# Kernel optimization log

Hardware: AMD Instinct MI355X
Metric: run time of the kernel (lower is better)

Reference implementation:

```python
import jax, jax.numpy as jnp
import numpy as np

TAG_SIZE = 50
START = TAG_SIZE - 2  # index of '<START>'
STOP = TAG_SIZE - 1   # index of '<STOP>'
B, S = 64, 512


def setup_inputs() -> dict:
    key = jax.random.key(0)
    k1, k2, k3 = jax.random.split(key, 3)
    feats = jax.random.normal(k1, (B, S, TAG_SIZE), dtype=jnp.float32)
    mask = jnp.ones((B, S), dtype=jnp.int32)
    tags = jax.random.randint(k2, (B, S), 0, START)  # valid tags exclude START/STOP
    transitions = jax.random.normal(k3, (TAG_SIZE, TAG_SIZE), dtype=jnp.float32)
    return {"feats": feats, "mask": mask, "tags": tags, "transitions": transitions}


def reference(feats, mask, tags, transitions):
    """CRF neg_log_likelihood_loss = forward_score (log partition, summed) - gold_score.
    feats: (B,S,T) emissions; mask: (B,S) {0,1}; tags: (B,S) gold tags;
    transitions[i,j] = score of transitioning from tag i to tag j.
    """
    b, s, t = feats.shape
    maskf = mask.astype(feats.dtype)

    # ---- forward algorithm (log partition) via scan over time ----
    feats_t = jnp.swapaxes(feats, 0, 1)            # (S,B,T)
    mask_t = jnp.swapaxes(mask, 0, 1).astype(bool)  # (S,B)
    # t=0: partition[b,j] = feats[b,0,j] + transitions[START, j]
    partition0 = feats_t[0] + transitions[START][None, :]  # (B,T)

    def step(partition, xs):
        f_t, m_t = xs  # (B,T), (B,)
        # cur_values[b,i,j] = partition[b,i] + transitions[i,j] + feats[b,t,j]
        cur_values = partition[:, :, None] + transitions[None, :, :] + f_t[:, None, :]
        cur = jax.nn.logsumexp(cur_values, axis=1)  # (B,T) logsumexp over prev tag
        new_partition = jnp.where(m_t[:, None], cur, partition)
        return new_partition, None

    partition, _ = jax.lax.scan(step, partition0, (feats_t[1:], mask_t[1:]))
    terminal = jax.nn.logsumexp(partition[:, :, None] + transitions[None, :, :], axis=1)  # (B,T)
    forward_score = terminal[:, STOP].sum()

    # ---- gold score ----
    # prev tag at step 0 is START, otherwise tags[:, t-1]
    prev = jnp.concatenate([jnp.full((b, 1), START, dtype=tags.dtype), tags[:, :-1]], axis=1)
    emit = jnp.take_along_axis(feats, tags[..., None], axis=2)[..., 0]  # (B,S)
    trans = transitions[prev, tags]                                      # (B,S)
    tg_energy = ((emit + trans) * maskf).sum()
    lengths = mask.astype(jnp.int32).sum(axis=1)                         # (B,)
    end_ids = jnp.take_along_axis(tags, (lengths - 1)[:, None].astype(tags.dtype), axis=1)[:, 0]
    end_energy = transitions[end_ids, STOP].sum()
    gold_score = tg_energy + end_energy

    return forward_score - gold_score
```

## Files before the change

### kernel.cpp

```cpp
#include <hip/hip_runtime.h>
#include <hip/hip_bf16.h>

#define T 50
#define NB 64
#define NS 512
#define START_TAG 48
#define STOP_TAG 49

typedef _Float16 f16_t;
typedef _Float16 f16x2 __attribute__((ext_vector_type(2)));
typedef _Float16 f16x4 __attribute__((ext_vector_type(4)));
typedef float    f32x4 __attribute__((ext_vector_type(4)));

static constexpr float LOG2E = 1.4426950408889634f;
static constexpr float LN2F  = 0.6931471805599453f;
static constexpr float S_E   = 6.0f;
#define NEG_BIG (-1.0e38f)

__device__ __forceinline__ float fexp2(float x) { return __builtin_amdgcn_exp2f(x); }
__device__ __forceinline__ float flog2(float x) { return __builtin_amdgcn_logf(x); }
__device__ __forceinline__ f16x2 bcast_h2(f16x2 v, int src) {
    unsigned u = __builtin_amdgcn_readlane(__builtin_bit_cast(unsigned, v), src);
    return __builtin_bit_cast(f16x2, u);
}
__device__ __forceinline__ f16x2 pack_h2(float a, float b) {
    return __builtin_bit_cast(f16x2, __builtin_amdgcn_cvt_pkrtz(a, b));
}

__device__ __forceinline__ float wave_fmax_dpp(float x) {
#define DPP_STEP(ctrl)                                                        \
    do {                                                                      \
        int _s = __builtin_bit_cast(int, x);                                  \
        int _p = __builtin_amdgcn_update_dpp(_s, _s, (ctrl), 0xf, 0xf, false);\
        x = fmaxf(x, __builtin_bit_cast(float, _p));                          \
    } while (0)
    DPP_STEP(0x111);
    DPP_STEP(0x112);
    DPP_STEP(0x114);
    DPP_STEP(0x118);
    DPP_STEP(0x142);
    DPP_STEP(0x143);
#undef DPP_STEP
    return __builtin_bit_cast(float,
        __builtin_amdgcn_readlane(__builtin_bit_cast(int, x), 63));
}

template<int NCHT, int CHLT>
__global__ __launch_bounds__(256, 6)
void crf_chunk(const float* __restrict__ feats, const int* __restrict__ mask,
               const float* __restrict__ trans, f16_t* __restrict__ wsCt,
               float* __restrict__ wsD, float* __restrict__ out, int out_size) {
    const int c    = blockIdx.x;
    const int b    = blockIdx.y;
    const int tid  = threadIdx.x;
    const int w    = tid >> 6;
    const int lane = tid & 63;
    const int l15  = lane & 15;
    const int q    = lane >> 4;

    __shared__ float sF[CHLT][64];
    __shared__ f16_t Ml[64 * 72];

    const int t0  = c * CHLT + 1;
    const int nst = (NS - t0 < CHLT) ? (NS - t0) : CHLT;

    f16x4 Afrag[4][4];
    #pragma unroll
    for (int mb = 0; mb < 4; mb++)
        #pragma unroll
        for (int kb = 0; kb < 4; kb++) {
            f16x4 v;
            #pragma unroll
            for (int j = 0; j < 4; j++) {
                const int kk = 16 * kb + 4 * q + j;
                const int mm = 16 * mb + l15;
                float x = 0.f;
                if (kk < T && mm < T) x = fexp2(fmaf(trans[kk * T + mm], LOG2E, -S_E));
                v[j] = (f16_t)x;
            }
            Afrag[mb][kb] = v;
        }

    for (int r = w; r < CHLT; r += 4) {
        int tl = t0 + r; tl = tl < NS ? tl : NS - 1;
        float fv = (lane < T && r < nst) ? feats[((size_t)b * NS + tl) * T + lane] : 0.f;
        sF[r][lane] = (lane < T && r < nst) ? fexp2(fv * LOG2E) : 0.f;
    }

    unsigned long long bm;
    {
        int tl = t0 + lane; tl = tl < NS ? tl : NS - 1;
        int mv = (lane < nst) ? mask[b * NS + tl] : 0;
        bm = __ballot(mv != 0);
    }
    __syncthreads();

    f16x4 Bt[4];
    #pragma unroll
    for (int rb = 0; rb < 4; rb++) {
        f16x4 v;
        #pragma unroll
        for (int j = 0; j < 4; j++)
            v[j] = (f16_t)((rb == w && 4 * q + j == l15) ? 1.f : 0.f);
        Bt[rb] = v;
    }

    float D  = 0.f;
    float m1 = 1.f, m2 = 1.f;

    for (int s = 0; s < nst; s++) {
        if ((bm >> s) & 1ull) {
            int ebits = (int)((__float_as_uint(m2) >> 23) & 255) - 127;
            ebits = ebits > 14 ? 14 : (ebits < -14 ? -14 : ebits);
            const float descale = __uint_as_float((unsigned)(127 - ebits) << 23);
            D += (float)ebits + S_E;

            const f32x4 zz = {0.f, 0.f, 0.f, 0.f};
            f32x4 acc[4];
            #pragma unroll
            for (int mb = 0; mb < 4; mb++)
                acc[mb] = __builtin_amdgcn_mfma_f32_16x16x16f16(Afrag[mb][0], Bt[0], zz, 0, 0, 0);
            #pragma unroll
            for (int kb = 1; kb < 4; kb++)
                #pragma unroll
                for (int mb = 0; mb < 4; mb++)
                    acc[mb] = __builtin_amdgcn_mfma_f32_16x16x16f16(Afrag[mb][kb], Bt[kb], acc[mb], 0, 0, 0);

            f16x2 wmax2 = {(f16_t)0.f, (f16_t)0.f};
            #pragma unroll
            for (int mb = 0; mb < 4; mb++) {
                f32x4 cs = *(const f32x4*)&sF[s][16 * mb + 4 * q];
                float v0 = acc[mb][0] * (cs[0] * descale);
                float v1 = acc[mb][1] * (cs[1] * descale);
                float v2 = acc[mb][2] * (cs[2] * descale);
                float v3 = acc[mb][3] * (cs[3] * descale);
                f16x4 hv;
                hv[0] = (f16_t)v0; hv[1] = (f16_t)v1;
                hv[2] = (f16_t)v2; hv[3] = (f16_t)v3;
                Bt[mb] = hv;
                f16x2 lo = __builtin_shufflevector(hv, hv, 0, 1);
                f16x2 hi = __builtin_shufflevector(hv, hv, 2, 3);
                wmax2 = __builtin_elementwise_max(wmax2,
                          __builtin_elementwise_max(lo, hi));
            }
            float wm = fmaxf((float)wmax2[0], (float)wmax2[1]);

            m2 = m1;
            m1 = wave_fmax_dpp(wm);
        }
    }

    {
        const int P2 = 72;
        #pragma unroll
        for (int rb = 0; rb < 4; rb++) {
            f16x4 v = Bt[rb];
            #pragma unroll
            for (int r = 0; r < 4; r++)
                Ml[(16 * rb + 4 * q + r) * P2 + 16 * w + l15] = v[r];
        }
        __syncthreads();
        const int row = tid >> 2;
        const int seg = tid & 3;
        const f16_t* src = &Ml[row * P2 + seg * 16];
        f16_t* dst = wsCt + ((size_t)(b * NCHT + c)) * 4096 + row * 64 + seg * 16;
        ((int4*)dst)[0] = *(const int4*)&src[0];
        ((int4*)dst)[1] = *(const int4*)&src[8];
    }
    if (lane == 0) wsD[(b * NCHT + c) * 4 + w] = D;

    if (c == 0 && b == 0 && tid < out_size) out[tid] = 0.f;
}

template<int NCHT>
__global__ __launch_bounds__(128, 1)
void crf_combine(const float* __restrict__ feats, const int* __restrict__ mask,
                 const int* __restrict__ tags, const float* __restrict__ trans,
                 const f16_t* __restrict__ wsCt, const float* __restrict__ wsD,
                 float* __restrict__ out) {
    const int b    = blockIdx.x;
    const int tid  = threadIdx.x;
    const int wv   = tid >> 6;
    const int lane = tid & 63;

    __shared__ float sGold;
    float fwd = 0.f;

    if (wv == 1) {
        float gsum = 0.f;
        int   lcnt = 0;
        for (int s = lane; s < NS; s += 64) {
            int   m  = mask[b * NS + s];
            int   tg = tags[b * NS + s];
            int   pv = (s == 0) ? START_TAG : tags[b * NS + s - 1];
            float e  = feats[((size_t)b * NS + s) * T + tg];
            float tr = trans[pv * T + tg];
            if (m) { gsum += e + tr; lcnt += 1; }
        }
        #pragma unroll
        for (int off = 32; off > 0; off >>= 1) {
            gsum += __shfl_down(gsum, off, 64);
            lcnt += __shfl_down(lcnt, off, 64);
        }
        if (lane == 0) sGold = gsum + trans[tags[b * NS + lcnt - 1] * T + STOP_TAG];
    } else {
        float part = (lane < T)
            ? (feats[(size_t)b * NS * T + lane] + trans[START_TAG * T + lane]) * LOG2E
            : NEG_BIG;

        float Dq[NCHT];
        #pragma unroll
        for (int cc = 0; cc < NCHT; cc++)
            Dq[cc] = wsD[(b * NCHT + cc) * 4 + (lane >> 4)];

        int bufA[32], bufB[32];
        {
            const f16_t* src = wsCt + (size_t)b * NCHT * 4096 + lane * 64;
            #pragma unroll
            for (int kk = 0; kk < 8; kk++)
                *(int4*)&bufA[4 * kk] = ((const int4*)src)[kk];
        }

        auto cbody = [&](int (&cur)[32], int (&nxt)[32], int cc) {
            if (cc + 1 < NCHT) {
                const f16_t* src = wsCt + (size_t)(b * NCHT + cc + 1) * 4096 + lane * 64;
                #pragma unroll
                for (int kk = 0; kk < 8; kk++)
                    *(int4*)&nxt[4 * kk] = ((const int4*)src)[kk];
            }

            float tmp = part + Dq[cc];
            float sft = wave_fmax_dpp(tmp);
            float ex  = fexp2(tmp - sft);
            float exo = __shfl_xor(ex, 1, 64);
            f16x2 pk  = pack_h2(ex, exo);

            float a0 = 0.f, a1 = 0.f, a2 = 0.f, a3 = 0.f;
            #pragma unroll
            for (int k = 0; k < 25; k += 4) {
                a0 = __builtin_amdgcn_fdot2(bcast_h2(pk, 2 * k), __builtin_bit_cast(f16x2, cur[k]), a0, false);
                if (k + 1 < 25) a1 = __builtin_amdgcn_fdot2(bcast_h2(pk, 2 * (k + 1)), __builtin_bit_cast(f16x2, cur[k + 1]), a1, false);
                if (k + 2 < 25) a2 = __builtin_amdgcn_fdot2(bcast_h2(pk, 2 * (k + 2)), __builtin_bit_cast(f16x2, cur[k + 2]), a2, false);
                if (k + 3 < 25) a3 = __builtin_amdgcn_fdot2(bcast_h2(pk, 2 * (k + 3)), __builtin_bit_cast(f16x2, cur[k + 3]), a3, false);
            }
            part = sft + flog2((a0 + a1) + (a2 + a3));
        };

        #pragma unroll
        for (int pp = 0; pp < NCHT / 2; pp++) {
            cbody(bufA, bufB, 2 * pp);
            cbody(bufB, bufA, 2 * pp + 1);
        }

        float v = (lane < T) ? part + trans[lane * T + STOP_TAG] * LOG2E : NEG_BIG;
        float mx = wave_fmax_dpp(v);
        float ee = (lane < T) ? fexp2(v - mx) : 0.f;
        #pragma unroll
        for (int off = 32; off > 0; off >>= 1) ee += __shfl_xor(ee, off, 64);
        fwd = (mx + flog2(ee)) * LN2F;
    }

    __syncthreads();
    if (tid == 0) atomicAdd(out, fwd - sGold);
}

extern "C" void kernel_launch(void* const* d_in, const int* in_sizes, int n_in,
                              void* d_out, int out_size, void* d_ws, size_t ws_size,
                              hipStream_t stream) {
    const float* feats = (const float*)d_in[0];
    const int*   mask  = (const int*)d_in[1];
    const int*   tags  = (const int*)d_in[2];
    const float* trans = (const float*)d_in[3];
    float* out = (float*)d_out;


    const size_t matBytes16 = (size_t)NB * 16 * 4096 * sizeof(f16_t);
    const size_t need16     = matBytes16 + (size_t)NB * 16 * 4 * sizeof(float);

    if (ws_size >= need16) {
        f16_t* wsCt = (f16_t*)d_ws;
        float* wsD  = (float*)((char*)d_ws + matBytes16);
        crf_chunk<16, 32><<<dim3(16, NB), 256, 0, stream>>>(feats, mask, trans, wsCt, wsD, out, out_size);
        crf_combine<16><<<NB, 128, 0, stream>>>(feats, mask, tags, trans, wsCt, wsD, out);
    } else {
        const size_t matBytes8 = (size_t)NB * 8 * 4096 * sizeof(f16_t);
        f16_t* wsCt = (f16_t*)d_ws;
        float* wsD  = (float*)((char*)d_ws + matBytes8);
        crf_chunk<8, 64><<<dim3(8, NB), 256, 0, stream>>>(feats, mask, trans, wsCt, wsD, out, out_size);
        crf_combine<8><<<NB, 128, 0, stream>>>(feats, mask, tags, trans, wsCt, wsD, out);
    }
}
```

Before: 106.5 us.

## Move transition MFMA fragments to LDS and triple-buffer chunk combine loads

The 16 register-resident A fragments of exp(transitions) move into a shared-memory buffer, and each step now reloads them as packed 8-wide LDS reads. This frees VGPRs so launch bounds can rise from 6 to 8 waves per SIMD. The shared buffer is reused for the final transpose, which needs an extra barrier. The chunk-combine phase switches from double to triple buffering of workspace loads to hide more global latency. The cost is eight LDS reads on the serial per-step MFMA chain, which adds latency to every timestep.

Measured after the change: 106.6 us. No clear change (+0.0%).

```diff
diff --git a/kernel.cpp b/kernel.cpp
--- a/kernel.cpp
+++ b/kernel.cpp
@@ -10,6 +10,7 @@
 typedef _Float16 f16_t;
 typedef _Float16 f16x2 __attribute__((ext_vector_type(2)));
 typedef _Float16 f16x4 __attribute__((ext_vector_type(4)));
+typedef _Float16 f16x8 __attribute__((ext_vector_type(8)));
 typedef float    f32x4 __attribute__((ext_vector_type(4)));
 
 static constexpr float LOG2E = 1.4426950408889634f;
@@ -46,7 +47,7 @@
 }
 
 template<int NCHT, int CHLT>
-__global__ __launch_bounds__(256, 6)
+__global__ __launch_bounds__(256, 8)
 void crf_chunk(const float* __restrict__ feats, const int* __restrict__ mask,
                const float* __restrict__ trans, f16_t* __restrict__ wsCt,
                float* __restrict__ wsD, float* __restrict__ out, int out_size) {
@@ -58,28 +59,36 @@
     const int l15  = lane & 15;
     const int q    = lane >> 4;
 
-    __shared__ float sF[CHLT][64];
-    __shared__ f16_t Ml[64 * 72];
+    constexpr int EF_BYTES = 4 * 2 * 64 * 16;
+    constexpr int SF_BYTES = CHLT * 64 * 4;
+    constexpr int ML_BYTES = 64 * 72 * 2;
+    constexpr int SM_BYTES = (EF_BYTES + SF_BYTES) > ML_BYTES
+                           ? (EF_BYTES + SF_BYTES) : ML_BYTES;
+    __shared__ unsigned char smem[SM_BYTES];
+    f16_t* Ef = (f16_t*)smem;
+    float (*sF)[64] = (float (*)[64])(smem + EF_BYTES);
 
     const int t0  = c * CHLT + 1;
     const int nst = (NS - t0 < CHLT) ? (NS - t0) : CHLT;
 
-    f16x4 Afrag[4][4];
-    #pragma unroll
-    for (int mb = 0; mb < 4; mb++)
-        #pragma unroll
-        for (int kb = 0; kb < 4; kb++) {
-            f16x4 v;
+    for (int sidx = tid; sidx < 512; sidx += 256) {
+        const int kb  = sidx >> 7;
+        const int mbp = (sidx >> 6) & 1;
+        const int ln  = sidx & 63;
+        const int qq  = ln >> 4;
+        const int ll  = ln & 15;
+        f16_t* slot = Ef + sidx * 8;
+        #pragma unroll
+        for (int e = 0; e < 2; e++)
             #pragma unroll
             for (int j = 0; j < 4; j++) {
-                const int kk = 16 * kb + 4 * q + j;
-                const int mm = 16 * mb + l15;
+                const int kk = 16 * kb + 4 * qq + j;
+                const int mm = 16 * (2 * mbp + e) + ll;
                 float x = 0.f;
                 if (kk < T && mm < T) x = fexp2(fmaf(trans[kk * T + mm], LOG2E, -S_E));
-                v[j] = (f16_t)x;
-            }
-            Afrag[mb][kb] = v;
-        }
+                slot[e * 4 + j] = (f16_t)x;
+            }
+    }
 
     for (int r = w; r < CHLT; r += 4) {
         int tl = t0 + r; tl = tl < NS ? tl : NS - 1;
@@ -107,6 +116,7 @@
 
     float D  = 0.f;
     float m1 = 1.f, m2 = 1.f;
+    const f16x8* EfL = (const f16x8*)Ef;
 
     for (int s = 0; s < nst; s++) {
         if ((bm >> s) & 1ull) {
@@ -117,14 +127,23 @@
 
             const f32x4 zz = {0.f, 0.f, 0.f, 0.f};
             f32x4 acc[4];
-            #pragma unroll
-            for (int mb = 0; mb < 4; mb++)
-                acc[mb] = __builtin_amdgcn_mfma_f32_16x16x16f16(Afrag[mb][0], Bt[0], zz, 0, 0, 0);
-            #pragma unroll
-            for (int kb = 1; kb < 4; kb++)
-                #pragma unroll
-                for (int mb = 0; mb < 4; mb++)
-                    acc[mb] = __builtin_amdgcn_mfma_f32_16x16x16f16(Afrag[mb][kb], Bt[kb], acc[mb], 0, 0, 0);
+            {
+                f16x8 p0 = EfL[0 * 64 + lane];
+                f16x8 p1 = EfL[1 * 64 + lane];
+                acc[0] = __builtin_amdgcn_mfma_f32_16x16x16f16(__builtin_shufflevector(p0, p0, 0,1,2,3), Bt[0], zz, 0, 0, 0);
+                acc[1] = __builtin_amdgcn_mfma_f32_16x16x16f16(__builtin_shufflevector(p0, p0, 4,5,6,7), Bt[0], zz, 0, 0, 0);
+                acc[2] = __builtin_amdgcn_mfma_f32_16x16x16f16(__builtin_shufflevector(p1, p1, 0,1,2,3), Bt[0], zz, 0, 0, 0);
+                acc[3] = __builtin_amdgcn_mfma_f32_16x16x16f16(__builtin_shufflevector(p1, p1, 4,5,6,7), Bt[0], zz, 0, 0, 0);
+            }
+            #pragma unroll
+            for (int kb = 1; kb < 4; kb++) {
+                f16x8 p0 = EfL[(kb * 2 + 0) * 64 + lane];
+                f16x8 p1 = EfL[(kb * 2 + 1) * 64 + lane];
+                acc[0] = __builtin_amdgcn_mfma_f32_16x16x16f16(__builtin_shufflevector(p0, p0, 0,1,2,3), Bt[kb], acc[0], 0, 0, 0);
+                acc[1] = __builtin_amdgcn_mfma_f32_16x16x16f16(__builtin_shufflevector(p0, p0, 4,5,6,7), Bt[kb], acc[1], 0, 0, 0);
+                acc[2] = __builtin_amdgcn_mfma_f32_16x16x16f16(__builtin_shufflevector(p1, p1, 0,1,2,3), Bt[kb], acc[2], 0, 0, 0);
+                acc[3] = __builtin_amdgcn_mfma_f32_16x16x16f16(__builtin_shufflevector(p1, p1, 4,5,6,7), Bt[kb], acc[3], 0, 0, 0);
+            }
 
             f16x2 wmax2 = {(f16_t)0.f, (f16_t)0.f};
             #pragma unroll
@@ -150,7 +169,9 @@
         }
     }
 
+    __syncthreads();
     {
+        f16_t* Ml = (f16_t*)smem;
         const int P2 = 72;
         #pragma unroll
         for (int rb = 0; rb < 4; rb++) {
@@ -213,22 +234,16 @@
         for (int cc = 0; cc < NCHT; cc++)
             Dq[cc] = wsD[(b * NCHT + cc) * 4 + (lane >> 4)];
 
-        int bufA[32], bufB[32];
-        {
-            const f16_t* src = wsCt + (size_t)b * NCHT * 4096 + lane * 64;
+        int bX[32], bY[32], bZ[32];
+
+        auto ld = [&](int (&buf)[32], int cc) {
+            const f16_t* src = wsCt + (size_t)(b * NCHT + cc) * 4096 + lane * 64;
             #pragma unroll
             for (int kk = 0; kk < 8; kk++)
-                *(int4*)&bufA[4 * kk] = ((const int4*)src)[kk];
-        }
-
-        auto cbody = [&](int (&cur)[32], int (&nxt)[32], int cc) {
-            if (cc + 1 < NCHT) {
-                const f16_t* src = wsCt + (size_t)(b * NCHT + cc + 1) * 4096 + lane * 64;
-                #pragma unroll
-                for (int kk = 0; kk < 8; kk++)
-                    *(int4*)&nxt[4 * kk] = ((const int4*)src)[kk];
-            }
-
+                *(int4*)&buf[4 * kk] = ((const int4*)src)[kk];
+        };
+
+        auto body = [&](int (&cur)[32], int cc) {
             float tmp = part + Dq[cc];
             float sft = wave_fmax_dpp(tmp);
             float ex  = fexp2(tmp - sft);
@@ -246,10 +261,13 @@
             part = sft + flog2((a0 + a1) + (a2 + a3));
         };
 
-        #pragma unroll
-        for (int pp = 0; pp < NCHT / 2; pp++) {
-            cbody(bufA, bufB, 2 * pp);
-            cbody(bufB, bufA, 2 * pp + 1);
+        ld(bX, 0);
+        if (1 < NCHT) ld(bY, 1);
+        #pragma unroll
+        for (int g = 0; g < NCHT; g += 3) {
+            { if (g + 2 < NCHT) ld(bZ, g + 2); body(bX, g); }
+            if (g + 1 < NCHT) { if (g + 3 < NCHT) ld(bX, g + 3); body(bY, g + 1); }
+            if (g + 2 < NCHT) { if (g + 4 < NCHT) ld(bY, g + 4); body(bZ, g + 2); }
         }
 
         float v = (lane < T) ? part + trans[lane * T + STOP_TAG] * LOG2E : NEG_BIG;
```
